# Optimization experiments

Hardware: AMD Instinct MI355X
Metric: run time of the kernel (lower is better)

The kernel has to match this reference:

```python
import jax, jax.numpy as jnp
import numpy as np

D_Z, D_A = 128, 64
D = D_Z + D_A            # 192
H1, H2 = 512, 512
E, S = 16, 1
B, N = 64, 2048
LN_EPS = 1e-5


def mish(x):
    return x * jnp.tanh(jax.nn.softplus(x))


def layernorm(x, g, b):
    m = jnp.mean(x, axis=-1, keepdims=True)
    v = jnp.mean((x - m) ** 2, axis=-1, keepdims=True)
    return (x - m) * jax.lax.rsqrt(v + LN_EPS) * g + b


def setup_inputs() -> dict:
    key = jax.random.key(0)
    ks = jax.random.split(key, 12)
    inp = {
        "z": jax.random.normal(ks[0], (B, N, D_Z), jnp.float32),
        "a": jax.random.normal(ks[1], (B, N, D_A), jnp.float32),
        "phi": jax.random.normal(ks[2], (D, E, S), jnp.float32) / np.sqrt(D),
        # stacked per-expert params (vectorized over e)
        "W1": jax.random.normal(ks[3], (E, D, H1), jnp.float32) / np.sqrt(D),
        "b1": jnp.zeros((E, H1), jnp.float32),
        "g1": jnp.ones((E, H1), jnp.float32),
        "be1": jnp.zeros((E, H1), jnp.float32),
        "W2": jax.random.normal(ks[4], (E, H1, H2), jnp.float32) / np.sqrt(H1),
        "b2": jnp.zeros((E, H2), jnp.float32),
        "g2": jnp.ones((E, H2), jnp.float32),
        "be2": jnp.zeros((E, H2), jnp.float32),
        "W3": jax.random.normal(ks[5], (E, H2, D_Z), jnp.float32) / np.sqrt(H2),
        "b3": jnp.zeros((E, D_Z), jnp.float32),
    }
    return inp


def reference(z, a, phi, W1, b1, g1, be1, W2, b2, g2, be2, W3, b3):
    x = jnp.concatenate([z, a], axis=-1)                      # [B,N,D]
    weights = jnp.einsum('bnd,des->bnes', x, phi)             # [B,N,E,S]
    dispatch = jax.nn.softmax(weights, axis=1)                # over tokens N
    xin = jnp.einsum('bnes,bnd->besd', dispatch, x)           # [B,E,S,D]
    # batched per-expert MLP: NormedLinear -> NormedLinear -> Linear
    h = jnp.einsum('besd,edh->besh', xin, W1) + b1[None, :, None, :]
    h = mish(layernorm(h, g1[None, :, None, :], be1[None, :, None, :]))
    h = jnp.einsum('besh,ehk->besk', h, W2) + b2[None, :, None, :]
    h = mish(layernorm(h, g2[None, :, None, :], be2[None, :, None, :]))
    out_e = jnp.einsum('besk,ekz->besz', h, W3) + b3[None, :, None, :]
    expert_outputs = out_e.reshape(out_e.shape[0], E * S, D_Z)    # b (e s) z
    combine = jax.nn.softmax(weights.reshape(weights.shape[0], weights.shape[1], E * S), axis=-1)
    out = jnp.einsum('bnk,bkz->bnz', combine, expert_outputs)     # [B,N,d_z]
    return out
```

## Files before the change

### kernel.cpp

```cpp
#include <hip/hip_runtime.h>
#include <math.h>

#define BB 64
#define NN 2048
#define DZ 128
#define DA 64
#define DD 192
#define EE 16
#define HH 512
#define LN_EPS 1e-5f

typedef __attribute__((ext_vector_type(8))) short short8;
typedef __attribute__((ext_vector_type(4))) float f32x4;

__device__ __forceinline__ float mishf(float x) {
    float sp = (x > 20.f) ? x : log1pf(__expf(x));
    return x * tanhf(sp);
}

__device__ __forceinline__ unsigned short bf16_rne(float f) {
    unsigned u = __float_as_uint(f);
    return (unsigned short)((u + 0x7FFFu + ((u >> 16) & 1u)) >> 16);
}
__device__ __forceinline__ float bf16f(unsigned short h) {
    return __uint_as_float(((unsigned)h) << 16);
}

__device__ __forceinline__ void gload_lds16(const float* g, float* l) {
    __builtin_amdgcn_global_load_lds(
        (const __attribute__((address_space(1))) void*)g,
        (__attribute__((address_space(3))) void*)l, 16, 0, 0);
}

__global__ __launch_bounds__(256)
void k_phipack(const float* __restrict__ phi, unsigned short* __restrict__ ph,
               unsigned short* __restrict__ pl) {
    int idx = blockIdx.x * 256 + threadIdx.x;
    if (idx >= 6 * 64 * 8) return;
    int j = idx & 7, lane = (idx >> 3) & 63, kk = idx >> 9;
    int e = lane & 15, g = lane >> 4;
    int d = kk * 32 + g * 8 + j;
    float f = phi[d * EE + e];
    unsigned short h = bf16_rne(f);
    ph[idx] = h;
    pl[idx] = bf16_rne(f - bf16f(h));
}

__global__ __launch_bounds__(256)
void k_weights(const float* __restrict__ z, const float* __restrict__ a,
               const unsigned short* __restrict__ php,
               const unsigned short* __restrict__ plp,
               float* __restrict__ w) {
    int t = threadIdx.x;
    int wv = t >> 6, l = t & 63;
    long tokbase = ((long)blockIdx.x * 4 + wv) * 16;
    long tokA = tokbase + (l & 15);
    int g = l >> 4;

    short8 bh[6], bl[6], ah[6], al[6];
#pragma unroll
    for (int kk = 0; kk < 6; kk++) {
        bh[kk] = *(const short8*)(php + kk * 512 + l * 8);
        bl[kk] = *(const short8*)(plp + kk * 512 + l * 8);
    }
#pragma unroll
    for (int kk = 0; kk < 6; kk++) {
        int d0 = kk * 32 + g * 8;
        const float* src = (d0 < DZ) ? (z + tokA * DZ + d0)
                                     : (a + tokA * DA + (d0 - DZ));
        float4 v0 = ((const float4*)src)[0];
        float4 v1 = ((const float4*)src)[1];
        float f[8] = {v0.x, v0.y, v0.z, v0.w, v1.x, v1.y, v1.z, v1.w};
#pragma unroll
        for (int j = 0; j < 8; j++) {
            unsigned short h = bf16_rne(f[j]);
            ah[kk][j] = (short)h;
            al[kk][j] = (short)bf16_rne(f[j] - bf16f(h));
        }
    }

    f32x4 acc = {0.f, 0.f, 0.f, 0.f};
#pragma unroll
    for (int kk = 0; kk < 6; kk++)
        acc = __builtin_amdgcn_mfma_f32_16x16x32_bf16(ah[kk], bh[kk], acc, 0, 0, 0);
#pragma unroll
    for (int kk = 0; kk < 6; kk++)
        acc = __builtin_amdgcn_mfma_f32_16x16x32_bf16(al[kk], bh[kk], acc, 0, 0, 0);
#pragma unroll
    for (int kk = 0; kk < 6; kk++)
        acc = __builtin_amdgcn_mfma_f32_16x16x32_bf16(ah[kk], bl[kk], acc, 0, 0, 0);

    int e = l & 15;
#pragma unroll
    for (int r = 0; r < 4; r++) {
        long row = tokbase + g * 4 + r;
        w[row * EE + e] = acc[r];
    }
}

#define RSTR 17
__global__ __launch_bounds__(256)
void k_stats1(const float* __restrict__ w, float* __restrict__ lmax,
              float* __restrict__ lsum) {
    __shared__ float red[256 * RSTR];
    int b = blockIdx.y, c = blockIdx.x, t = threadIdx.x;
    const float* wb = w + ((long)b * NN + c * 512) * EE;

    float m[EE];
#pragma unroll
    for (int e = 0; e < EE; e++) m[e] = -1e30f;
    for (int k = 0; k < 2; k++) {
        const float4* row = (const float4*)(wb + ((long)(k * 256 + t)) * EE);
#pragma unroll
        for (int q = 0; q < 4; q++) {
            float4 v = row[q];
            m[q * 4 + 0] = fmaxf(m[q * 4 + 0], v.x);
            m[q * 4 + 1] = fmaxf(m[q * 4 + 1], v.y);
            m[q * 4 + 2] = fmaxf(m[q * 4 + 2], v.z);
            m[q * 4 + 3] = fmaxf(m[q * 4 + 3], v.w);
        }
    }
#pragma unroll
    for (int e = 0; e < EE; e++) red[t * RSTR + e] = m[e];
    __syncthreads();
    for (int s = 128; s > 0; s >>= 1) {
        if (t < s) {
#pragma unroll
            for (int e = 0; e < EE; e++)
                red[t * RSTR + e] = fmaxf(red[t * RSTR + e], red[(t + s) * RSTR + e]);
        }
        __syncthreads();
    }
    float mg[EE];
#pragma unroll
    for (int e = 0; e < EE; e++) mg[e] = red[e];
    __syncthreads();

    float s_[EE];
#pragma unroll
    for (int e = 0; e < EE; e++) s_[e] = 0.f;
    for (int k = 0; k < 2; k++) {
        const float4* row = (const float4*)(wb + ((long)(k * 256 + t)) * EE);
#pragma unroll
        for (int q = 0; q < 4; q++) {
            float4 v = row[q];
            s_[q * 4 + 0] += __expf(v.x - mg[q * 4 + 0]);
            s_[q * 4 + 1] += __expf(v.y - mg[q * 4 + 1]);
            s_[q * 4 + 2] += __expf(v.z - mg[q * 4 + 2]);
            s_[q * 4 + 3] += __expf(v.w - mg[q * 4 + 3]);
        }
    }
#pragma unroll
    for (int e = 0; e < EE; e++) red[t * RSTR + e] = s_[e];
    __syncthreads();
    for (int s = 128; s > 0; s >>= 1) {
        if (t < s) {
#pragma unroll
            for (int e = 0; e < EE; e++)
                red[t * RSTR + e] += red[(t + s) * RSTR + e];
        }
        __syncthreads();
    }
    if (t < EE) {
        lmax[((long)b * 4 + c) * EE + t] = mg[t];
        lsum[((long)b * 4 + c) * EE + t] = red[t];
    }
}

__global__ __launch_bounds__(256)
void k_stats2(const float* __restrict__ lmax, const float* __restrict__ lsum,
              float* __restrict__ gmax, float* __restrict__ grcp) {
    int idx = blockIdx.x * 256 + threadIdx.x;
    if (idx >= BB * EE) return;
    int b = idx >> 4, e = idx & 15;
    float gm = -1e30f;
#pragma unroll
    for (int c = 0; c < 4; c++)
        gm = fmaxf(gm, lmax[((long)b * 4 + c) * EE + e]);
    float Z = 0.f;
#pragma unroll
    for (int c = 0; c < 4; c++)
        Z += __expf(lmax[((long)b * 4 + c) * EE + e] - gm) * lsum[((long)b * 4 + c) * EE + e];
    gmax[idx] = gm;
    grcp[idx] = 1.f / Z;
}

__global__ __launch_bounds__(256)
void k_xin2(const float* __restrict__ z, const float* __restrict__ a,
            const float* __restrict__ w, const float* __restrict__ gmax,
            const float* __restrict__ grcp, float* __restrict__ pxin) {
    __shared__ float zs[2][32 * 128];
    __shared__ float as_[2][32 * 64];
    __shared__ float ws_[2][32 * 16];
    int kq = blockIdx.x, b = blockIdx.y;
    int t = threadIdx.x, wv = t >> 6, l = t & 63;
    int g = l >> 4, c = l & 15;

    float gm = gmax[b * EE + c];
    float gr = grcp[b * EE + c];
    const float* zb = z + ((long)b * NN + (long)kq * 128) * DZ;
    const float* ab = a + ((long)b * NN + (long)kq * 128) * DA;
    const float* wb = w + ((long)b * NN + (long)kq * 128) * EE;

    auto stage = [&](int kk, int bf) {
#pragma unroll
        for (int s = 0; s < 4; s++) {
            int seg = wv * 4 + s;
            gload_lds16(zb + kk * 4096 + seg * 256 + l * 4, &zs[bf][seg * 256]);
        }
#pragma unroll
        for (int s = 0; s < 2; s++) {
            int seg = wv * 2 + s;
            gload_lds16(ab + kk * 2048 + seg * 256 + l * 4, &as_[bf][seg * 256]);
        }
        if (wv < 2)
            gload_lds16(wb + kk * 512 + wv * 256 + l * 4, &ws_[bf][wv * 256]);
    };

    f32x4 acc0 = {0.f, 0.f, 0.f, 0.f};
    f32x4 acc1 = {0.f, 0.f, 0.f, 0.f};
    f32x4 acc2 = {0.f, 0.f, 0.f, 0.f};

    stage(0, 0);
#pragma unroll
    for (int kk = 0; kk < 4; kk++) {
        int bf = kk & 1;
        if (kk < 3) stage(kk + 1, bf ^ 1);
        __syncthreads();

        short8 ad;
#pragma unroll
        for (int j = 0; j < 8; j++) {
            float wvv = ws_[bf][(g * 8 + j) * 16 + c];
            ad[j] = (short)bf16_rne(__expf(wvv - gm) * gr);
        }
#pragma unroll
        for (int i = 0; i < 3; i++) {
            int d = (wv * 3 + i) * 16 + c;
            short8 xh_, xl_;
#pragma unroll
            for (int j = 0; j < 8; j++) {
                int n = g * 8 + j;
                float f = (d < DZ) ? zs[bf][n * 128 + d]
                                   : as_[bf][n * 64 + (d - DZ)];
                unsigned short h = bf16_rne(f);
                xh_[j] = (short)h;
                xl_[j] = (short)bf16_rne(f - bf16f(h));
            }
            if (i == 0) {
                acc0 = __builtin_amdgcn_mfma_f32_16x16x32_bf16(ad, xh_, acc0, 0, 0, 0);
                acc0 = __builtin_amdgcn_mfma_f32_16x16x32_bf16(ad, xl_, acc0, 0, 0, 0);
            } else if (i == 1) {
                acc1 = __builtin_amdgcn_mfma_f32_16x16x32_bf16(ad, xh_, acc1, 0, 0, 0);
                acc1 = __builtin_amdgcn_mfma_f32_16x16x32_bf16(ad, xl_, acc1, 0, 0, 0);
            } else {
                acc2 = __builtin_amdgcn_mfma_f32_16x16x32_bf16(ad, xh_, acc2, 0, 0, 0);
                acc2 = __builtin_amdgcn_mfma_f32_16x16x32_bf16(ad, xl_, acc2, 0, 0, 0);
            }
        }
        __syncthreads();
    }

    float* pb = pxin + (long)kq * (EE * BB * DD) + (long)b * DD;
#pragma unroll
    for (int r = 0; r < 4; r++) {
        int e = g * 4 + r;
        float* pr = pb + (long)e * (BB * DD);
        pr[(wv * 3 + 0) * 16 + c] = acc0[r];
        pr[(wv * 3 + 1) * 16 + c] = acc1[r];
        pr[(wv * 3 + 2) * 16 + c] = acc2[r];
    }
}

__global__ __launch_bounds__(192)
void k_xin_scalar(const float* __restrict__ z, const float* __restrict__ a,
                  const float* __restrict__ w, const float* __restrict__ gmax,
                  const float* __restrict__ grcp, float* __restrict__ dst) {
    __shared__ float disp[128 * EE];
    int b = blockIdx.y, chunk = blockIdx.x, t = threadIdx.x;

    const float* wrow = w + ((long)b * NN + (long)chunk * 128) * EE;
    for (int i = t; i < 128 * EE; i += 192) {
        int e = i & 15;
        disp[i] = __expf(wrow[i] - gmax[b * EE + e]) * grcp[b * EE + e];
    }
    __syncthreads();

    const float* xp;
    int stride;
    if (t < DZ) { xp = z + ((long)b * NN + (long)chunk * 128) * DZ + t; stride = DZ; }
    else        { xp = a + ((long)b * NN + (long)chunk * 128) * DA + (t - DZ); stride = DA; }

    float acc[EE];
#pragma unroll
    for (int e = 0; e < EE; e++) acc[e] = 0.f;

    for (int n = 0; n < 128; n++) {
        float xv = xp[(long)n * stride];
        const float4* dp = (const float4*)(disp + n * EE);
#pragma unroll
        for (int q = 0; q < 4; q++) {
            float4 p = dp[q];
            acc[q * 4 + 0] += p.x * xv;
            acc[q * 4 + 1] += p.y * xv;
            acc[q * 4 + 2] += p.z * xv;
            acc[q * 4 + 3] += p.w * xv;
        }
    }
#pragma unroll
    for (int e = 0; e < EE; e++)
        atomicAdd(&dst[((long)e * BB + b) * DD + t], acc[e]);
}

__global__ __launch_bounds__(256)
void k_xinred(const float* __restrict__ xinp, float* __restrict__ xin) {
    long i = (long)blockIdx.x * 256 + threadIdx.x;
    float s = 0.f;
#pragma unroll
    for (int c = 0; c < 16; c++)
        s += xinp[(long)c * (EE * BB * DD) + i];
    xin[i] = s;
}

template<int K, int OUT, int KSLICE, bool ADD_BIAS>
__global__ __launch_bounds__(256)
void k_gemm(const float* __restrict__ X, const float* __restrict__ W,
            const float* __restrict__ bias, float* __restrict__ Yp) {
    constexpr int SP = KSLICE + 4;
    constexpr int K4 = KSLICE / 4;
    __shared__ float xs[64 * SP];

    int cb = blockIdx.x, ks = blockIdx.y, e = blockIdx.z;
    int t = threadIdx.x;
    int k0 = ks * KSLICE;

    for (int i = t; i < 64 * K4; i += 256) {
        int r = i / K4, k4 = i % K4;
        *(float4*)&xs[r * SP + k4 * 4] =
            *(const float4*)(X + ((long)e * BB + r) * K + k0 + k4 * 4);
    }
    __syncthreads();

    int c = cb * 32 + (t & 7) * 4;
    int r0 = (t >> 3) * 2;
    const float* Wp = W + ((long)e * K + k0) * OUT + c;

    float acc0[4], acc1[4];
#pragma unroll
    for (int j = 0; j < 4; j++) {
        float bv = ADD_BIAS ? bias[(long)e * OUT + c + j] : 0.f;
        acc0[j] = bv;
        acc1[j] = bv;
    }

#pragma unroll 4
    for (int k4 = 0; k4 < K4; k4++) {
        float4 x0 = *(const float4*)&xs[r0 * SP + k4 * 4];
        float4 x1 = *(const float4*)&xs[(r0 + 1) * SP + k4 * 4];
        const float* xp0 = &x0.x;
        const float* xp1 = &x1.x;
#pragma unroll
        for (int j = 0; j < 4; j++) {
            float4 wv = *(const float4*)(Wp + (long)(k4 * 4 + j) * OUT);
            float xa = xp0[j], xb = xp1[j];
            acc0[0] += xa * wv.x; acc0[1] += xa * wv.y;
            acc0[2] += xa * wv.z; acc0[3] += xa * wv.w;
            acc1[0] += xb * wv.x; acc1[1] += xb * wv.y;
            acc1[2] += xb * wv.z; acc1[3] += xb * wv.w;
        }
    }

    float* yp = Yp + ((long)ks * (EE * BB) + (long)e * BB + r0) * OUT + c;
    *(float4*)yp         = make_float4(acc0[0], acc0[1], acc0[2], acc0[3]);
    *(float4*)(yp + OUT) = make_float4(acc1[0], acc1[1], acc1[2], acc1[3]);
}

template<int KS, bool HAS_BIAS>
__global__ __launch_bounds__(256)
void k_lnact(const float* __restrict__ Yp, const float* __restrict__ bias,
             const float* __restrict__ g, const float* __restrict__ be,
             float* __restrict__ Yo) {
    __shared__ float redS[4], redQ[4];
    int row = blockIdx.x, t = threadIdx.x;
    int e = row >> 6;

    float v[2];
#pragma unroll
    for (int j = 0; j < 2; j++) {
        int cj = t + j * 256;
        float s = HAS_BIAS ? bias[(long)e * HH + cj] : 0.f;
#pragma unroll
        for (int ks = 0; ks < KS; ks++)
            s += Yp[((long)ks * (EE * BB) + row) * HH + cj];
        v[j] = s;
    }
    float s = v[0] + v[1];
    float q = v[0] * v[0] + v[1] * v[1];
    for (int off = 32; off > 0; off >>= 1) {
        s += __shfl_xor(s, off);
        q += __shfl_xor(q, off);
    }
    int wave = t >> 6, lane = t & 63;
    if (lane == 0) { redS[wave] = s; redQ[wave] = q; }
    __syncthreads();
    float S = redS[0] + redS[1] + redS[2] + redS[3];
    float Q = redQ[0] + redQ[1] + redQ[2] + redQ[3];
    float mean = S * (1.f / HH);
    float var = Q * (1.f / HH) - mean * mean;
    float rstd = rsqrtf(var + LN_EPS);

#pragma unroll
    for (int j = 0; j < 2; j++) {
        int cj = t + j * 256;
        float gg = g[(long)e * HH + cj], bb = be[(long)e * HH + cj];
        Yo[(long)row * HH + cj] = mishf((v[j] - mean) * rstd * gg + bb);
    }
}

template<int KS>
__global__ __launch_bounds__(256)
void k_fin3(const float* __restrict__ p3, const float* __restrict__ b3,
            float* __restrict__ eout) {
    int t = threadIdx.x;
    int row = blockIdx.x * 2 + (t >> 7);
    int c = t & 127;
    int e = row >> 6, b = row & 63;
    float s = b3[(long)e * DZ + c];
#pragma unroll
    for (int ks = 0; ks < KS; ks++)
        s += p3[((long)ks * (EE * BB) + row) * DZ + c];
    eout[((long)b * EE + e) * DZ + c] = s;
}

__global__ __launch_bounds__(256)
void k_combine(const float* __restrict__ w, const float* __restrict__ eout,
               float* __restrict__ out) {
    __shared__ float comb[64][EE];
    __shared__ float eo[EE * DZ];
    int b = blockIdx.y, n0 = blockIdx.x * 64, t = threadIdx.x;

    for (int i = t; i < EE * DZ; i += 256) eo[i] = eout[(long)b * EE * DZ + i];

    int tok = t >> 2, sub = t & 3;
    const float4 wv = *(const float4*)(w + ((long)b * NN + n0 + tok) * EE + sub * 4);
    float mx = fmaxf(fmaxf(wv.x, wv.y), fmaxf(wv.z, wv.w));
    mx = fmaxf(mx, __shfl_xor(mx, 1, 4));
    mx = fmaxf(mx, __shfl_xor(mx, 2, 4));
    float e0 = __expf(wv.x - mx), e1 = __expf(wv.y - mx);
    float e2 = __expf(wv.z - mx), e3 = __expf(wv.w - mx);
    float s = e0 + e1 + e2 + e3;
    s += __shfl_xor(s, 1, 4);
    s += __shfl_xor(s, 2, 4);
    float rs = 1.f / s;
    comb[tok][sub * 4 + 0] = e0 * rs;
    comb[tok][sub * 4 + 1] = e1 * rs;
    comb[tok][sub * 4 + 2] = e2 * rs;
    comb[tok][sub * 4 + 3] = e3 * rs;
    __syncthreads();

    for (int i = t; i < 64 * DZ; i += 256) {
        int tk = i >> 7, c = i & 127;
        float acc = 0.f;
#pragma unroll
        for (int e = 0; e < EE; e++) acc += comb[tk][e] * eo[e * DZ + c];
        out[((long)b * NN + n0 + tk) * DZ + c] = acc;
    }
}

extern "C" void kernel_launch(void* const* d_in, const int* in_sizes, int n_in,
                              void* d_out, int out_size, void* d_ws, size_t ws_size,
                              hipStream_t stream) {
    const float* z   = (const float*)d_in[0];
    const float* a   = (const float*)d_in[1];
    const float* phi = (const float*)d_in[2];
    const float* W1  = (const float*)d_in[3];
    const float* b1  = (const float*)d_in[4];
    const float* g1  = (const float*)d_in[5];
    const float* be1 = (const float*)d_in[6];
    const float* W2  = (const float*)d_in[7];
    const float* b2  = (const float*)d_in[8];
    const float* g2  = (const float*)d_in[9];
    const float* be2 = (const float*)d_in[10];
    const float* W3  = (const float*)d_in[11];
    const float* b3  = (const float*)d_in[12];
    float* out = (float*)d_out;

    char* p = (char*)d_ws;
    float* w    = (float*)p; p += (size_t)BB * NN * EE * 4;
    float* gmax = (float*)p; p += (size_t)BB * EE * 4;
    float* grcp = (float*)p; p += (size_t)BB * EE * 4;
    float* lmax = (float*)p; p += (size_t)BB * 4 * EE * 4;
    float* lsum = (float*)p; p += (size_t)BB * 4 * EE * 4;
    float* xin  = (float*)p; p += (size_t)BB * EE * DD * 4;
    unsigned short* php = (unsigned short*)p; p += 6 * 64 * 8 * 2;
    unsigned short* plp = (unsigned short*)p; p += 6 * 64 * 8 * 2;
    char* region = p;
    float* pxin = (float*)region;
    float* part = (float*)region;
    float* h1   = (float*)(region + (size_t)4 * EE * BB * HH * 4);
    float* h2   = h1;
    float* eout = (float*)(region + (size_t)4 * EE * BB * HH * 4
                                  + (size_t)EE * BB * HH * 4);
    size_t region_off = (size_t)(region - (char*)d_ws);
    size_t need_full = region_off + (size_t)16 * EE * BB * DD * 4;
    bool full = ws_size >= need_full;

    k_phipack<<<12, 256, 0, stream>>>(phi, php, plp);
    k_weights<<<BB * NN / 64, 256, 0, stream>>>(z, a, php, plp, w);
    k_stats1<<<dim3(4, BB), 256, 0, stream>>>(w, lmax, lsum);
    k_stats2<<<4, 256, 0, stream>>>(lmax, lsum, gmax, grcp);

    if (full) {
        k_xin2<<<dim3(16, BB), 256, 0, stream>>>(z, a, w, gmax, grcp, pxin);
        k_xinred<<<EE * BB * DD / 256, 256, 0, stream>>>(pxin, xin);
    } else {
        hipMemsetAsync(xin, 0, (size_t)BB * EE * DD * 4, stream);
        k_xin_scalar<<<dim3(NN / 128, BB), 192, 0, stream>>>(z, a, w, gmax, grcp, xin);
    }

    k_gemm<DD, HH, 96, false>
        <<<dim3(HH / 32, 2, EE), 256, 0, stream>>>(xin, W1, nullptr, part);
    k_lnact<2, true><<<EE * BB, 256, 0, stream>>>(part, b1, g1, be1, h1);

    k_gemm<HH, HH, 128, false>
        <<<dim3(HH / 32, 4, EE), 256, 0, stream>>>(h1, W2, nullptr, part);
    k_lnact<4, true><<<EE * BB, 256, 0, stream>>>(part, b2, g2, be2, h2);

    k_gemm<HH, DZ, 64, false>
        <<<dim3(DZ / 32, 8, EE), 256, 0, stream>>>(h2, W3, nullptr, part);
    k_fin3<8><<<EE * BB / 2, 256, 0, stream>>>(part, b3, eout);

    k_combine<<<dim3(NN / 64, BB), 256, 0, stream>>>(w, eout, out);
}
```

Baseline: 134.6 us.

## Fold softmax stats finalize into xin kernel, pad LDS segments, trim syncs

The k_stats2 launch is removed on the main path. Each k_xin2 thread now rebuilds the global max and reciprocal sum from the per-chunk lmax/lsum partials, which saves a launch and a small global round trip at the cost of a few redundant loads and exps per thread. The z, a and w LDS staging buffers are padded per 256-float segment to reduce bank conflicts on the strided column reads. The per-iteration barrier after staging is replaced by one barrier before the loop, relying on the end-of-iteration barrier to make the next buffer visible.

Result: no change. 135.5 us (+0.6%).

```diff
diff --git a/kernel.cpp b/kernel.cpp
--- a/kernel.cpp
+++ b/kernel.cpp
@@ -185,19 +185,31 @@
     grcp[idx] = 1.f / Z;
 }
 
+#define SEGZ 260
+#define SEGA 260
+#define SEGW 272
 __global__ __launch_bounds__(256)
 void k_xin2(const float* __restrict__ z, const float* __restrict__ a,
-            const float* __restrict__ w, const float* __restrict__ gmax,
-            const float* __restrict__ grcp, float* __restrict__ pxin) {
-    __shared__ float zs[2][32 * 128];
-    __shared__ float as_[2][32 * 64];
-    __shared__ float ws_[2][32 * 16];
+            const float* __restrict__ w, const float* __restrict__ lmax,
+            const float* __restrict__ lsum, float* __restrict__ pxin) {
+    __shared__ float zs[2][16 * SEGZ];
+    __shared__ float as_[2][8 * SEGA];
+    __shared__ float ws_[2][2 * SEGW];
     int kq = blockIdx.x, b = blockIdx.y;
     int t = threadIdx.x, wv = t >> 6, l = t & 63;
     int g = l >> 4, c = l & 15;
 
-    float gm = gmax[b * EE + c];
-    float gr = grcp[b * EE + c];
+    float gm = -1e30f;
+#pragma unroll
+    for (int cc = 0; cc < 4; cc++)
+        gm = fmaxf(gm, lmax[((long)b * 4 + cc) * EE + c]);
+    float Zs = 0.f;
+#pragma unroll
+    for (int cc = 0; cc < 4; cc++)
+        Zs += __expf(lmax[((long)b * 4 + cc) * EE + c] - gm)
+            * lsum[((long)b * 4 + cc) * EE + c];
+    float gr = 1.f / Zs;
+
     const float* zb = z + ((long)b * NN + (long)kq * 128) * DZ;
     const float* ab = a + ((long)b * NN + (long)kq * 128) * DA;
     const float* wb = w + ((long)b * NN + (long)kq * 128) * EE;
@@ -206,15 +218,15 @@
 #pragma unroll
         for (int s = 0; s < 4; s++) {
             int seg = wv * 4 + s;
-            gload_lds16(zb + kk * 4096 + seg * 256 + l * 4, &zs[bf][seg * 256]);
+            gload_lds16(zb + kk * 4096 + seg * 256 + l * 4, &zs[bf][seg * SEGZ]);
         }
 #pragma unroll
         for (int s = 0; s < 2; s++) {
             int seg = wv * 2 + s;
-            gload_lds16(ab + kk * 2048 + seg * 256 + l * 4, &as_[bf][seg * 256]);
+            gload_lds16(ab + kk * 2048 + seg * 256 + l * 4, &as_[bf][seg * SEGA]);
         }
         if (wv < 2)
-            gload_lds16(wb + kk * 512 + wv * 256 + l * 4, &ws_[bf][wv * 256]);
+            gload_lds16(wb + kk * 512 + wv * 256 + l * 4, &ws_[bf][wv * SEGW]);
     };
 
     f32x4 acc0 = {0.f, 0.f, 0.f, 0.f};
@@ -222,16 +234,17 @@
     f32x4 acc2 = {0.f, 0.f, 0.f, 0.f};
 
     stage(0, 0);
+    __syncthreads();
 #pragma unroll
     for (int kk = 0; kk < 4; kk++) {
         int bf = kk & 1;
         if (kk < 3) stage(kk + 1, bf ^ 1);
-        __syncthreads();
 
         short8 ad;
 #pragma unroll
         for (int j = 0; j < 8; j++) {
-            float wvv = ws_[bf][(g * 8 + j) * 16 + c];
+            int n = g * 8 + j;
+            float wvv = ws_[bf][(n >> 4) * SEGW + (n & 15) * 16 + c];
             ad[j] = (short)bf16_rne(__expf(wvv - gm) * gr);
         }
 #pragma unroll
@@ -241,8 +254,9 @@
 #pragma unroll
             for (int j = 0; j < 8; j++) {
                 int n = g * 8 + j;
-                float f = (d < DZ) ? zs[bf][n * 128 + d]
-                                   : as_[bf][n * 64 + (d - DZ)];
+                float f = (d < DZ)
+                    ? zs[bf][(n >> 1) * SEGZ + (n & 1) * 128 + d]
+                    : as_[bf][(n >> 2) * SEGA + (n & 3) * 64 + (d - DZ)];
                 unsigned short h = bf16_rne(f);
                 xh_[j] = (short)h;
                 xl_[j] = (short)bf16_rne(f - bf16f(h));
@@ -508,12 +522,12 @@
     k_phipack<<<12, 256, 0, stream>>>(phi, php, plp);
     k_weights<<<BB * NN / 64, 256, 0, stream>>>(z, a, php, plp, w);
     k_stats1<<<dim3(4, BB), 256, 0, stream>>>(w, lmax, lsum);
-    k_stats2<<<4, 256, 0, stream>>>(lmax, lsum, gmax, grcp);
 
     if (full) {
-        k_xin2<<<dim3(16, BB), 256, 0, stream>>>(z, a, w, gmax, grcp, pxin);
+        k_xin2<<<dim3(16, BB), 256, 0, stream>>>(z, a, w, lmax, lsum, pxin);
         k_xinred<<<EE * BB * DD / 256, 256, 0, stream>>>(pxin, xin);
     } else {
+        k_stats2<<<4, 256, 0, stream>>>(lmax, lsum, gmax, grcp);
         hipMemsetAsync(xin, 0, (size_t)BB * EE * DD * 4, stream);
         k_xin_scalar<<<dim3(NN / 128, BB), 192, 0, stream>>>(z, a, w, gmax, grcp, xin);
     }
```
